# Kernel tuning notes

Measured on AMD Instinct MI355X. Metric: run time of the kernel, lower is better.

Reference implementation:

```python
import jax, jax.numpy as jnp
import numpy as np

N_NODES = 100000
N_EDGES = 3200000
IN_CH = 128
HID_CH = 128   # 2 * out_channels
OUT_CH = 64


def setup_inputs() -> dict:
    key = jax.random.key(0)
    ks = jax.random.split(key, 6)
    x = jax.random.normal(ks[0], (N_NODES, IN_CH), dtype=jnp.float32)
    edge_index = jax.random.randint(ks[1], (2, N_EDGES), 0, N_NODES, dtype=jnp.int64)
    # Glorot-ish init for GCN linear weights
    W1 = jax.random.normal(ks[2], (IN_CH, HID_CH), dtype=jnp.float32) / np.sqrt(IN_CH)
    b1 = jnp.zeros((HID_CH,), dtype=jnp.float32)
    W2 = jax.random.normal(ks[3], (HID_CH, OUT_CH), dtype=jnp.float32) / np.sqrt(HID_CH)
    b2 = jnp.zeros((OUT_CH,), dtype=jnp.float32)
    return {"x": x, "edge_index": edge_index, "W1": W1, "b1": b1, "W2": W2, "b2": b2}


def gcn_conv(x, src, dst, W, b, n):
    """PyG GCNConv: add self-loops, symmetric D^-1/2 (A+I) D^-1/2 normalization,
    linear transform, scatter-add aggregation, then bias."""
    h = x @ W  # [N, C_out]
    ones = jnp.ones(src.shape[0], dtype=x.dtype)
    deg = jax.ops.segment_sum(ones, dst, num_segments=n) + 1.0  # self-loop degree
    dinv = jax.lax.rsqrt(deg)  # [N]
    coef = dinv[src] * dinv[dst]  # [E] edge normalization
    agg = jax.ops.segment_sum(h[src] * coef[:, None], dst, num_segments=n)
    agg = agg + h * (dinv * dinv)[:, None]  # self-loop contribution
    return agg + b


def reference(x, edge_index, W1, b1, W2, b2):
    src, dst = edge_index[0], edge_index[1]
    n = x.shape[0]
    h = jax.nn.relu(gcn_conv(x, src, dst, W1, b1, n))
    out = jax.nn.relu(gcn_conv(h, src, dst, W2, b2, n))
    return out
```

## Files before the change

### kernel.cpp

```cpp
#include <hip/hip_runtime.h>
#include <hip/hip_fp16.h>
#include <cstdint>
#include <cstddef>


#define BSHIFT 8

typedef _Float16 half8 __attribute__((ext_vector_type(8)));
typedef float f32x4 __attribute__((ext_vector_type(4)));

__global__ __launch_bounds__(256) void k_hist(const int* __restrict__ dst,
                                              int* __restrict__ bkthist, int E) {
  __shared__ int h[512];
  for (int t = threadIdx.x; t < 512; t += 256) h[t] = 0;
  __syncthreads();
  int i = blockIdx.x * 256 + threadIdx.x;
  const int stride = gridDim.x * 256;
  for (; i < E; i += stride) atomicAdd(&h[dst[i] >> BSHIFT], 1);
  __syncthreads();
  for (int t = threadIdx.x; t < 512; t += 256)
    if (h[t]) atomicAdd(&bkthist[t], h[t]);
}

__global__ __launch_bounds__(256) void k_bktscan(const int* __restrict__ bkthist,
                                                 int* __restrict__ bktbase,
                                                 int* __restrict__ bktcur,
                                                 int* __restrict__ offsets, int n,
                                                 int E, int nbkt) {
  __shared__ int sc[512];
  const int t = threadIdx.x;
  sc[t] = (t < nbkt) ? bkthist[t] : 0;
  sc[256 + t] = (256 + t < nbkt) ? bkthist[256 + t] : 0;
  __syncthreads();
  if (t == 0) {
    int run = 0;
    for (int b = 0; b < nbkt; ++b) {
      const int c = sc[b];
      sc[b] = run;
      run += c;
    }
    offsets[n] = E;
    bktbase[nbkt] = E;
  }
  __syncthreads();
  if (t < nbkt) {
    bktbase[t] = sc[t];
    bktcur[t] = sc[t];
  }
  if (256 + t < nbkt) {
    bktbase[256 + t] = sc[256 + t];
    bktcur[256 + t] = sc[256 + t];
  }
}

__global__ __launch_bounds__(256) void k_part(const int* __restrict__ src,
                                              const int* __restrict__ dst,
                                              int* __restrict__ bktcur,
                                              int* __restrict__ part, int E,
                                              int nbkt) {
  __shared__ int hist[512];
  const int tid = threadIdx.x;
  const int e0 = blockIdx.x * 4096;
  for (int b = tid; b < nbkt; b += 256) hist[b] = 0;
  __syncthreads();
#pragma unroll
  for (int j = 0; j < 16; ++j) {
    const int e = e0 + j * 256 + tid;
    if (e < E) atomicAdd(&hist[dst[e] >> BSHIFT], 1);
  }
  __syncthreads();
  for (int b = tid; b < nbkt; b += 256) {
    const int c = hist[b];
    hist[b] = c ? atomicAdd(&bktcur[b], c) : 0;
  }
  __syncthreads();
#pragma unroll
  for (int j = 0; j < 16; ++j) {
    const int e = e0 + j * 256 + tid;
    if (e < E) {
      const int d = dst[e];
      const int pos = atomicAdd(&hist[d >> BSHIFT], 1);
      part[pos] = (src[e] << BSHIFT) | (d & ((1 << BSHIFT) - 1));
    }
  }
}

__global__ __launch_bounds__(256) void k_csr2(const int* __restrict__ part,
                                              const int* __restrict__ bktbase,
                                              int* __restrict__ offsets,
                                              int* __restrict__ csr_src,
                                              float* __restrict__ dinv, int n) {
  __shared__ int cnt[256];
  __shared__ int ts[256];
  const int b = blockIdx.x;
  const int node0 = b << BSHIFT;
  const int nn = min(256, n - node0);
  const int t = threadIdx.x;
  cnt[t] = 0;
  __syncthreads();
  const int w0 = bktbase[b];
  const int w1 = bktbase[b + 1];
  for (int e = w0 + t; e < w1; e += 256)
    atomicAdd(&cnt[part[e] & ((1 << BSHIFT) - 1)], 1);
  __syncthreads();
  const int c = cnt[t];
  ts[t] = c;
  __syncthreads();
  for (int off = 1; off < 256; off <<= 1) {
    const int u = (t >= off) ? ts[t - off] : 0;
    __syncthreads();
    ts[t] += u;
    __syncthreads();
  }
  const int excl = ts[t] - c;
  if (t < nn) {
    offsets[node0 + t] = w0 + excl;
    dinv[node0 + t] = rsqrtf((float)c + 1.0f);
  }
  cnt[t] = w0 + excl;
  __syncthreads();
  for (int e = w0 + t; e < w1; e += 256) {
    const int p = part[e];
    const int pos = atomicAdd(&cnt[p & ((1 << BSHIFT) - 1)], 1);
    csr_src[pos] = p >> BSHIFT;
  }
}

template <typename TA, int COLS>
__global__ __launch_bounds__(256) void k_gemm_mfma(const TA* __restrict__ A,
                                                   const float* __restrict__ W,
                                                   __half* __restrict__ Hout,
                                                   int N, int ntiles) {
  constexpr int RW = (COLS == 128) ? 2 : 4;
  constexpr int RPT = RW * 16;
  __shared__ _Float16 Wt[128 * COLS];
  __shared__ _Float16 Lb[4][16][72];
  const int tid = threadIdx.x;
  const int w = tid >> 6;
  const int l = tid & 63;

  for (int f = tid; f < (128 * COLS) / 4; f += 256) {
    const int k = f / (COLS / 4);
    const int c4 = (f % (COLS / 4)) * 4;
    const float4 wv = *reinterpret_cast<const float4*>(W + (size_t)k * COLS + c4);
#pragma unroll
    for (int j = 0; j < 4; ++j) {
      const int cc = c4 + j;
      Wt[(cc * 128 + k) ^ ((cc & 7) << 3)] = (_Float16)(&wv.x)[j];
    }
  }
  __syncthreads();

  const int colw = (COLS == 128) ? (w >> 1) * 64 : 0;
  const int rw = (COLS == 128) ? (w & 1) : w;
  const int koff = (l >> 4) * 8;

  half8 bf[4][4];
#pragma unroll
  for (int t = 0; t < 4; ++t)
#pragma unroll
    for (int s = 0; s < 4; ++s) {
      const int cc = colw + 16 * t + (l & 15);
      const int kk = 32 * s + koff;
      bf[t][s] =
          *reinterpret_cast<const half8*>(&Wt[(cc * 128 + kk) ^ ((cc & 7) << 3)]);
    }

  for (int tile = blockIdx.x; tile < ntiles; tile += gridDim.x) {
    const int row = tile * RPT + rw * 16 + (l & 15);
    const int rowc = (row < N) ? row : (N - 1);
    f32x4 acc[4];
#pragma unroll
    for (int t = 0; t < 4; ++t) acc[t] = (f32x4){0.f, 0.f, 0.f, 0.f};

#pragma unroll
    for (int s = 0; s < 4; ++s) {
      half8 af;
      if constexpr (sizeof(TA) == 4) {
        const float* ap = (const float*)A + (size_t)rowc * 128 + 32 * s + koff;
        const float4 a0 = *reinterpret_cast<const float4*>(ap);
        const float4 a1 = *reinterpret_cast<const float4*>(ap + 4);
#pragma unroll
        for (int j = 0; j < 4; ++j) {
          af[j] = (_Float16)(&a0.x)[j];
          af[4 + j] = (_Float16)(&a1.x)[j];
        }
      } else {
        af = *reinterpret_cast<const half8*>((const __half*)A +
                                             (size_t)rowc * 128 + 32 * s + koff);
      }
#pragma unroll
      for (int t = 0; t < 4; ++t)
        acc[t] = __builtin_amdgcn_mfma_f32_16x16x32_f16(af, bf[t][s], acc[t],
                                                        0, 0, 0);
    }

#pragma unroll
    for (int t = 0; t < 4; ++t)
#pragma unroll
      for (int r = 0; r < 4; ++r)
        Lb[w][(l >> 4) * 4 + r][16 * t + (l & 15)] = (_Float16)acc[t][r];
    const int orow = tile * RPT + rw * 16 + (l & 15);
    if (orow < N) {
      const int ch = (l >> 4) * 16;
      const half8 v0 = *reinterpret_cast<const half8*>(&Lb[w][l & 15][ch]);
      const half8 v1 = *reinterpret_cast<const half8*>(&Lb[w][l & 15][ch + 8]);
      __half* hp = Hout + (size_t)orow * COLS + colw + ch;
      *reinterpret_cast<half8*>(hp) = v0;
      *reinterpret_cast<half8*>(hp + 8) = v1;
    }
  }
}

__global__ __launch_bounds__(256) void k_gather128(
    const __half* __restrict__ H, const int* __restrict__ offsets,
    const int* __restrict__ csr_src, const float* __restrict__ dinv,
    const float* __restrict__ bias, float* __restrict__ out, int N) {
  const int lane = threadIdx.x & 63;
  const int g = lane >> 3;
  const int sl = lane & 7;
  int w = (blockIdx.x * 256 + threadIdx.x) >> 6;
  const int nw = (gridDim.x * 256) >> 6;
  for (int i = w; i < N; i += nw) {
    const float di = dinv[i];
    const int beg = offsets[i];
    const int end = offsets[i + 1];
    float acc[16];
    {
      const float cfs = (g == 0) ? di * di : 0.f;
      const float4 ha = *reinterpret_cast<const float4*>(H + (size_t)i * 128 + sl * 16);
      const float4 hb = *reinterpret_cast<const float4*>(H + (size_t)i * 128 + sl * 16 + 8);
      const __half2* hpa = reinterpret_cast<const __half2*>(&ha);
      const __half2* hpb = reinterpret_cast<const __half2*>(&hb);
#pragma unroll
      for (int q = 0; q < 4; ++q) {
        const float2 fa = __half22float2(hpa[q]);
        const float2 fb = __half22float2(hpb[q]);
        acc[q * 2] = cfs * fa.x;
        acc[q * 2 + 1] = cfs * fa.y;
        acc[8 + q * 2] = cfs * fb.x;
        acc[8 + q * 2 + 1] = cfs * fb.y;
      }
    }
    for (int base = beg; base < end; base += 8) {
      const int e = base + g;
      const bool v = e < end;
      const int s = v ? csr_src[e] : i;
      const float cf = v ? dinv[s] * di : 0.f;
      const float4 ha = *reinterpret_cast<const float4*>(H + (size_t)s * 128 + sl * 16);
      const float4 hb = *reinterpret_cast<const float4*>(H + (size_t)s * 128 + sl * 16 + 8);
      const __half2* hpa = reinterpret_cast<const __half2*>(&ha);
      const __half2* hpb = reinterpret_cast<const __half2*>(&hb);
#pragma unroll
      for (int q = 0; q < 4; ++q) {
        const float2 fa = __half22float2(hpa[q]);
        const float2 fb = __half22float2(hpb[q]);
        acc[q * 2] = fmaf(cf, fa.x, acc[q * 2]);
        acc[q * 2 + 1] = fmaf(cf, fa.y, acc[q * 2 + 1]);
        acc[8 + q * 2] = fmaf(cf, fb.x, acc[8 + q * 2]);
        acc[8 + q * 2 + 1] = fmaf(cf, fb.y, acc[8 + q * 2 + 1]);
      }
    }
#pragma unroll
    for (int j = 0; j < 16; ++j) {
      float a = acc[j];
      a += __shfl_xor(a, 8);
      a += __shfl_xor(a, 16);
      a += __shfl_xor(a, 32);
      acc[j] = a;
    }
    if (g == 0) {
      float* op = out + (size_t)i * 128 + sl * 16;
      const float4 b0 = *reinterpret_cast<const float4*>(bias + sl * 16);
      const float4 b1 = *reinterpret_cast<const float4*>(bias + sl * 16 + 4);
      const float4 b2 = *reinterpret_cast<const float4*>(bias + sl * 16 + 8);
      const float4 b3 = *reinterpret_cast<const float4*>(bias + sl * 16 + 12);
      float4 o;
      o.x = fmaxf(acc[0] + b0.x, 0.f);
      o.y = fmaxf(acc[1] + b0.y, 0.f);
      o.z = fmaxf(acc[2] + b0.z, 0.f);
      o.w = fmaxf(acc[3] + b0.w, 0.f);
      *reinterpret_cast<float4*>(op) = o;
      o.x = fmaxf(acc[4] + b1.x, 0.f);
      o.y = fmaxf(acc[5] + b1.y, 0.f);
      o.z = fmaxf(acc[6] + b1.z, 0.f);
      o.w = fmaxf(acc[7] + b1.w, 0.f);
      *reinterpret_cast<float4*>(op + 4) = o;
      o.x = fmaxf(acc[8] + b2.x, 0.f);
      o.y = fmaxf(acc[9] + b2.y, 0.f);
      o.z = fmaxf(acc[10] + b2.z, 0.f);
      o.w = fmaxf(acc[11] + b2.w, 0.f);
      *reinterpret_cast<float4*>(op + 8) = o;
      o.x = fmaxf(acc[12] + b3.x, 0.f);
      o.y = fmaxf(acc[13] + b3.y, 0.f);
      o.z = fmaxf(acc[14] + b3.z, 0.f);
      o.w = fmaxf(acc[15] + b3.w, 0.f);
      *reinterpret_cast<float4*>(op + 12) = o;
    }
  }
}

__global__ __launch_bounds__(256) void k_gather64(
    const __half* __restrict__ H, const int* __restrict__ offsets,
    const int* __restrict__ csr_src, const float* __restrict__ dinv,
    const float* __restrict__ bias, float* __restrict__ out, int N) {
  const int lane = threadIdx.x & 63;
  const int g = lane >> 3;
  const int sl = lane & 7;
  int w = (blockIdx.x * 256 + threadIdx.x) >> 6;
  const int nw = (gridDim.x * 256) >> 6;
  for (int i = w; i < N; i += nw) {
    const float di = dinv[i];
    const int beg = offsets[i];
    const int end = offsets[i + 1];
    float acc[8];
    {
      const float cfs = (g == 0) ? di * di : 0.f;
      const float4 ha = *reinterpret_cast<const float4*>(H + (size_t)i * 64 + sl * 8);
      const __half2* hpa = reinterpret_cast<const __half2*>(&ha);
#pragma unroll
      for (int q = 0; q < 4; ++q) {
        const float2 fa = __half22float2(hpa[q]);
        acc[q * 2] = cfs * fa.x;
        acc[q * 2 + 1] = cfs * fa.y;
      }
    }
    for (int base = beg; base < end; base += 8) {
      const int e = base + g;
      const bool v = e < end;
      const int s = v ? csr_src[e] : i;
      const float cf = v ? dinv[s] * di : 0.f;
      const float4 ha = *reinterpret_cast<const float4*>(H + (size_t)s * 64 + sl * 8);
      const __half2* hpa = reinterpret_cast<const __half2*>(&ha);
#pragma unroll
      for (int q = 0; q < 4; ++q) {
        const float2 fa = __half22float2(hpa[q]);
        acc[q * 2] = fmaf(cf, fa.x, acc[q * 2]);
        acc[q * 2 + 1] = fmaf(cf, fa.y, acc[q * 2 + 1]);
      }
    }
#pragma unroll
    for (int j = 0; j < 8; ++j) {
      float a = acc[j];
      a += __shfl_xor(a, 8);
      a += __shfl_xor(a, 16);
      a += __shfl_xor(a, 32);
      acc[j] = a;
    }
    if (g == 0) {
      float* op = out + (size_t)i * 64 + sl * 8;
      const float4 b0 = *reinterpret_cast<const float4*>(bias + sl * 8);
      const float4 b1 = *reinterpret_cast<const float4*>(bias + sl * 8 + 4);
      float4 o;
      o.x = fmaxf(acc[0] + b0.x, 0.f);
      o.y = fmaxf(acc[1] + b0.y, 0.f);
      o.z = fmaxf(acc[2] + b0.z, 0.f);
      o.w = fmaxf(acc[3] + b0.w, 0.f);
      *reinterpret_cast<float4*>(op) = o;
      o.x = fmaxf(acc[4] + b1.x, 0.f);
      o.y = fmaxf(acc[5] + b1.y, 0.f);
      o.z = fmaxf(acc[6] + b1.z, 0.f);
      o.w = fmaxf(acc[7] + b1.w, 0.f);
      *reinterpret_cast<float4*>(op + 4) = o;
    }
  }
}

extern "C" void kernel_launch(void* const* d_in, const int* in_sizes, int n_in,
                              void* d_out, int out_size, void* d_ws,
                              size_t ws_size, hipStream_t stream) {
  const float* x  = (const float*)d_in[0];
  const int*   ei = (const int*)d_in[1];
  const float* W1 = (const float*)d_in[2];
  const float* b1 = (const float*)d_in[3];
  const float* W2 = (const float*)d_in[4];
  const float* b2 = (const float*)d_in[5];

  const int IN  = 128;
  const int n   = in_sizes[0] / IN;
  const int E   = in_sizes[1] / 2;
  const int HID = in_sizes[2] / IN;
  const int* srcv = ei;
  const int* dstv = ei + E;
  float* out = (float*)d_out;

  const int NBKT = (n + 255) >> BSHIFT;
  const int NCHK = (E + 4095) / 4096;
  const int NT1  = (n + 31) / 32;
  const int NT2  = (n + 63) / 64;

  char* p = (char*)d_ws;
  auto take = [&](size_t bytes) {
    char* r = p;
    p += (bytes + 255) & ~(size_t)255;
    return r;
  };
  float*  dinv    = (float*)take((size_t)n * 4);
  int*    offsets = (int*)take((size_t)(n + 1) * 4);
  int*    bkthist = (int*)take(512 * 4);
  int*    bktbase = (int*)take(512 * 4);
  int*    bktcur  = (int*)take(512 * 4);
  int*    csr_src = (int*)take((size_t)E * 4);
  __half* H16     = (__half*)take((size_t)n * 128 * 2);
  float*  bufHp   = (float*)take((size_t)n * HID * 4);
  int*    part    = (int*)bufHp;

  hipMemsetAsync(bkthist, 0, 512 * 4, stream);
  k_hist<<<1024, 256, 0, stream>>>(dstv, bkthist, E);
  k_bktscan<<<1, 256, 0, stream>>>(bkthist, bktbase, bktcur, offsets, n, E, NBKT);
  k_part<<<NCHK, 256, 0, stream>>>(srcv, dstv, bktcur, part, E, NBKT);
  k_csr2<<<NBKT, 256, 0, stream>>>(part, bktbase, offsets, csr_src, dinv, n);

  k_gemm_mfma<float, 128><<<512, 256, 0, stream>>>(x, W1, H16, n, NT1);
  k_gather128<<<25000, 256, 0, stream>>>(H16, offsets, csr_src, dinv, b1,
                                         bufHp, n);

  k_gemm_mfma<float, 64><<<512, 256, 0, stream>>>(bufHp, W2, H16, n, NT2);
  k_gather64<<<25000, 256, 0, stream>>>(H16, offsets, csr_src, dinv, b2,
                                        out, n);
}
```

Baseline: 360.7 us.

## Slice H into column-sliced planes so gather blocks each touch one slice

```diff
diff --git a/kernel.cpp b/kernel.cpp
--- a/kernel.cpp
+++ b/kernel.cpp
@@ -8,6 +8,7 @@
 
 typedef _Float16 half8 __attribute__((ext_vector_type(8)));
 typedef float f32x4 __attribute__((ext_vector_type(4)));
+struct alignas(8) h4 { __half2 a, b; };
 
 __global__ __launch_bounds__(256) void k_hist(const int* __restrict__ dst,
                                               int* __restrict__ bkthist, int E) {
@@ -129,7 +130,7 @@
 template <typename TA, int COLS>
 __global__ __launch_bounds__(256) void k_gemm_mfma(const TA* __restrict__ A,
                                                    const float* __restrict__ W,
-                                                   __half* __restrict__ Hout,
+                                                   __half* __restrict__ Hs,
                                                    int N, int ntiles) {
   constexpr int RW = (COLS == 128) ? 2 : 4;
   constexpr int RPT = RW * 16;
@@ -205,163 +206,79 @@
       const int ch = (l >> 4) * 16;
       const half8 v0 = *reinterpret_cast<const half8*>(&Lb[w][l & 15][ch]);
       const half8 v1 = *reinterpret_cast<const half8*>(&Lb[w][l & 15][ch + 8]);
-      __half* hp = Hout + (size_t)orow * COLS + colw + ch;
-      *reinterpret_cast<half8*>(hp) = v0;
-      *reinterpret_cast<half8*>(hp + 8) = v1;
-    }
-  }
-}
-
-__global__ __launch_bounds__(256) void k_gather128(
-    const __half* __restrict__ H, const int* __restrict__ offsets,
+      const int cb = colw + ch;
+      if constexpr (COLS == 128) {
+        __half* hp = Hs + (size_t)(cb >> 4) * N * 16 + (size_t)orow * 16;
+        *reinterpret_cast<half8*>(hp) = v0;
+        *reinterpret_cast<half8*>(hp + 8) = v1;
+      } else {
+        __half* hp0 = Hs + (size_t)(cb >> 3) * N * 8 + (size_t)orow * 8;
+        __half* hp1 = Hs + (size_t)((cb >> 3) + 1) * N * 8 + (size_t)orow * 8;
+        *reinterpret_cast<half8*>(hp0) = v0;
+        *reinterpret_cast<half8*>(hp1) = v1;
+      }
+    }
+  }
+}
+
+template <int LPE, int COLS>
+__global__ __launch_bounds__(256) void k_gather_sl(
+    const __half* __restrict__ Hs, const int* __restrict__ offsets,
     const int* __restrict__ csr_src, const float* __restrict__ dinv,
     const float* __restrict__ bias, float* __restrict__ out, int N) {
+  constexpr int CH = LPE * 4;
+  constexpr int GPE = 64 / LPE;
+  const int sidx = blockIdx.x & 7;
+  const __half* Hb = Hs + (size_t)sidx * N * CH;
   const int lane = threadIdx.x & 63;
-  const int g = lane >> 3;
-  const int sl = lane & 7;
-  int w = (blockIdx.x * 256 + threadIdx.x) >> 6;
-  const int nw = (gridDim.x * 256) >> 6;
+  const int g = lane / LPE;
+  const int cl = lane % LPE;
+  const int c0 = sidx * CH + cl * 4;
+  int w = (blockIdx.x >> 3) * 4 + (threadIdx.x >> 6);
+  const int nw = (gridDim.x >> 3) * 4;
   for (int i = w; i < N; i += nw) {
     const float di = dinv[i];
     const int beg = offsets[i];
     const int end = offsets[i + 1];
-    float acc[16];
+    float acc[4];
     {
       const float cfs = (g == 0) ? di * di : 0.f;
-      const float4 ha = *reinterpret_cast<const float4*>(H + (size_t)i * 128 + sl * 16);
-      const float4 hb = *reinterpret_cast<const float4*>(H + (size_t)i * 128 + sl * 16 + 8);
-      const __half2* hpa = reinterpret_cast<const __half2*>(&ha);
-      const __half2* hpb = reinterpret_cast<const __half2*>(&hb);
-#pragma unroll
-      for (int q = 0; q < 4; ++q) {
-        const float2 fa = __half22float2(hpa[q]);
-        const float2 fb = __half22float2(hpb[q]);
-        acc[q * 2] = cfs * fa.x;
-        acc[q * 2 + 1] = cfs * fa.y;
-        acc[8 + q * 2] = cfs * fb.x;
-        acc[8 + q * 2 + 1] = cfs * fb.y;
-      }
-    }
-    for (int base = beg; base < end; base += 8) {
+      const h4 hv = *reinterpret_cast<const h4*>(Hb + (size_t)i * CH + cl * 4);
+      const float2 fa = __half22float2(hv.a);
+      const float2 fb = __half22float2(hv.b);
+      acc[0] = cfs * fa.x;
+      acc[1] = cfs * fa.y;
+      acc[2] = cfs * fb.x;
+      acc[3] = cfs * fb.y;
+    }
+    for (int base = beg; base < end; base += GPE) {
       const int e = base + g;
       const bool v = e < end;
-      const int s = v ? csr_src[e] : i;
+      const int s = v ? __builtin_nontemporal_load(csr_src + e) : i;
       const float cf = v ? dinv[s] * di : 0.f;
-      const float4 ha = *reinterpret_cast<const float4*>(H + (size_t)s * 128 + sl * 16);
-      const float4 hb = *reinterpret_cast<const float4*>(H + (size_t)s * 128 + sl * 16 + 8);
-      const __half2* hpa = reinterpret_cast<const __half2*>(&ha);
-      const __half2* hpb = reinterpret_cast<const __half2*>(&hb);
-#pragma unroll
-      for (int q = 0; q < 4; ++q) {
-        const float2 fa = __half22float2(hpa[q]);
-        const float2 fb = __half22float2(hpb[q]);
-        acc[q * 2] = fmaf(cf, fa.x, acc[q * 2]);
-        acc[q * 2 + 1] = fmaf(cf, fa.y, acc[q * 2 + 1]);
-        acc[8 + q * 2] = fmaf(cf, fb.x, acc[8 + q * 2]);
-        acc[8 + q * 2 + 1] = fmaf(cf, fb.y, acc[8 + q * 2 + 1]);
-      }
-    }
-#pragma unroll
-    for (int j = 0; j < 16; ++j) {
+      const h4 hv = *reinterpret_cast<const h4*>(Hb + (size_t)s * CH + cl * 4);
+      const float2 fa = __half22float2(hv.a);
+      const float2 fb = __half22float2(hv.b);
+      acc[0] = fmaf(cf, fa.x, acc[0]);
+      acc[1] = fmaf(cf, fa.y, acc[1]);
+      acc[2] = fmaf(cf, fb.x, acc[2]);
+      acc[3] = fmaf(cf, fb.y, acc[3]);
+    }
+#pragma unroll
+    for (int j = 0; j < 4; ++j) {
       float a = acc[j];
-      a += __shfl_xor(a, 8);
-      a += __shfl_xor(a, 16);
-      a += __shfl_xor(a, 32);
+#pragma unroll
+      for (int off = LPE; off < 64; off <<= 1) a += __shfl_xor(a, off);
       acc[j] = a;
     }
     if (g == 0) {
-      float* op = out + (size_t)i * 128 + sl * 16;
-      const float4 b0 = *reinterpret_cast<const float4*>(bias + sl * 16);
-      const float4 b1 = *reinterpret_cast<const float4*>(bias + sl * 16 + 4);
-      const float4 b2 = *reinterpret_cast<const float4*>(bias + sl * 16 + 8);
-      const float4 b3 = *reinterpret_cast<const float4*>(bias + sl * 16 + 12);
+      const float4 bv = *reinterpret_cast<const float4*>(bias + c0);
       float4 o;
-      o.x = fmaxf(acc[0] + b0.x, 0.f);
-      o.y = fmaxf(acc[1] + b0.y, 0.f);
-      o.z = fmaxf(acc[2] + b0.z, 0.f);
-      o.w = fmaxf(acc[3] + b0.w, 0.f);
-      *reinterpret_cast<float4*>(op) = o;
-      o.x = fmaxf(acc[4] + b1.x, 0.f);
-      o.y = fmaxf(acc[5] + b1.y, 0.f);
-      o.z = fmaxf(acc[6] + b1.z, 0.f);
-      o.w = fmaxf(acc[7] + b1.w, 0.f);
-      *reinterpret_cast<float4*>(op + 4) = o;
-      o.x = fmaxf(acc[8] + b2.x, 0.f);
-      o.y = fmaxf(acc[9] + b2.y, 0.f);
-      o.z = fmaxf(acc[10] + b2.z, 0.f);
-      o.w = fmaxf(acc[11] + b2.w, 0.f);
-      *reinterpret_cast<float4*>(op + 8) = o;
-      o.x = fmaxf(acc[12] + b3.x, 0.f);
-      o.y = fmaxf(acc[13] + b3.y, 0.f);
-      o.z = fmaxf(acc[14] + b3.z, 0.f);
-      o.w = fmaxf(acc[15] + b3.w, 0.f);
-      *reinterpret_cast<float4*>(op + 12) = o;
-    }
-  }
-}
-
-__global__ __launch_bounds__(256) void k_gather64(
-    const __half* __restrict__ H, const int* __restrict__ offsets,
-    const int* __restrict__ csr_src, const float* __restrict__ dinv,
-    const float* __restrict__ bias, float* __restrict__ out, int N) {
-  const int lane = threadIdx.x & 63;
-  const int g = lane >> 3;
-  const int sl = lane & 7;
-  int w = (blockIdx.x * 256 + threadIdx.x) >> 6;
-  const int nw = (gridDim.x * 256) >> 6;
-  for (int i = w; i < N; i += nw) {
-    const float di = dinv[i];
-    const int beg = offsets[i];
-    const int end = offsets[i + 1];
-    float acc[8];
-    {
-      const float cfs = (g == 0) ? di * di : 0.f;
-      const float4 ha = *reinterpret_cast<const float4*>(H + (size_t)i * 64 + sl * 8);
-      const __half2* hpa = reinterpret_cast<const __half2*>(&ha);
-#pragma unroll
-      for (int q = 0; q < 4; ++q) {
-        const float2 fa = __half22float2(hpa[q]);
-        acc[q * 2] = cfs * fa.x;
-        acc[q * 2 + 1] = cfs * fa.y;
-      }
-    }
-    for (int base = beg; base < end; base += 8) {
-      const int e = base + g;
-      const bool v = e < end;
-      const int s = v ? csr_src[e] : i;
-      const float cf = v ? dinv[s] * di : 0.f;
-      const float4 ha = *reinterpret_cast<const float4*>(H + (size_t)s * 64 + sl * 8);
-      const __half2* hpa = reinterpret_cast<const __half2*>(&ha);
-#pragma unroll
-      for (int q = 0; q < 4; ++q) {
-        const float2 fa = __half22float2(hpa[q]);
-        acc[q * 2] = fmaf(cf, fa.x, acc[q * 2]);
-        acc[q * 2 + 1] = fmaf(cf, fa.y, acc[q * 2 + 1]);
-      }
-    }
-#pragma unroll
-    for (int j = 0; j < 8; ++j) {
-      float a = acc[j];
-      a += __shfl_xor(a, 8);
-      a += __shfl_xor(a, 16);
-      a += __shfl_xor(a, 32);
-      acc[j] = a;
-    }
-    if (g == 0) {
-      float* op = out + (size_t)i * 64 + sl * 8;
-      const float4 b0 = *reinterpret_cast<const float4*>(bias + sl * 8);
-      const float4 b1 = *reinterpret_cast<const float4*>(bias + sl * 8 + 4);
-      float4 o;
-      o.x = fmaxf(acc[0] + b0.x, 0.f);
-      o.y = fmaxf(acc[1] + b0.y, 0.f);
-      o.z = fmaxf(acc[2] + b0.z, 0.f);
-      o.w = fmaxf(acc[3] + b0.w, 0.f);
-      *reinterpret_cast<float4*>(op) = o;
-      o.x = fmaxf(acc[4] + b1.x, 0.f);
-      o.y = fmaxf(acc[5] + b1.y, 0.f);
-      o.z = fmaxf(acc[6] + b1.z, 0.f);
-      o.w = fmaxf(acc[7] + b1.w, 0.f);
-      *reinterpret_cast<float4*>(op + 4) = o;
+      o.x = fmaxf(acc[0] + bv.x, 0.f);
+      o.y = fmaxf(acc[1] + bv.y, 0.f);
+      o.z = fmaxf(acc[2] + bv.z, 0.f);
+      o.w = fmaxf(acc[3] + bv.w, 0.f);
+      *reinterpret_cast<float4*>(out + (size_t)i * COLS + c0) = o;
     }
   }
 }
@@ -412,10 +329,10 @@
   k_csr2<<<NBKT, 256, 0, stream>>>(part, bktbase, offsets, csr_src, dinv, n);
 
   k_gemm_mfma<float, 128><<<512, 256, 0, stream>>>(x, W1, H16, n, NT1);
-  k_gather128<<<25000, 256, 0, stream>>>(H16, offsets, csr_src, dinv, b1,
-                                         bufHp, n);
+  k_gather_sl<4, 128><<<8192, 256, 0, stream>>>(H16, offsets, csr_src, dinv,
+                                                b1, bufHp, n);
 
   k_gemm_mfma<float, 64><<<512, 256, 0, stream>>>(bufHp, W2, H16, n, NT2);
-  k_gather64<<<25000, 256, 0, stream>>>(H16, offsets, csr_src, dinv, b2,
-                                        out, n);
-}
+  k_gather_sl<2, 64><<<8192, 256, 0, stream>>>(H16, offsets, csr_src, dinv,
+                                               b2, out, n);
+}
```

Result: slower. 985.9 us (+173.4%).

## Drop histogram pass via fixed-capacity buckets and store hidden activations in fp16

Applied to the files above, without the earlier changes.

```diff
diff --git a/kernel.cpp b/kernel.cpp
--- a/kernel.cpp
+++ b/kernel.cpp
@@ -5,52 +5,14 @@
 
 
 #define BSHIFT 8
+#define CAP    12288
 
 typedef _Float16 half8 __attribute__((ext_vector_type(8)));
 typedef float f32x4 __attribute__((ext_vector_type(4)));
 
-__global__ __launch_bounds__(256) void k_hist(const int* __restrict__ dst,
-                                              int* __restrict__ bkthist, int E) {
-  __shared__ int h[512];
-  for (int t = threadIdx.x; t < 512; t += 256) h[t] = 0;
-  __syncthreads();
-  int i = blockIdx.x * 256 + threadIdx.x;
-  const int stride = gridDim.x * 256;
-  for (; i < E; i += stride) atomicAdd(&h[dst[i] >> BSHIFT], 1);
-  __syncthreads();
-  for (int t = threadIdx.x; t < 512; t += 256)
-    if (h[t]) atomicAdd(&bkthist[t], h[t]);
-}
-
-__global__ __launch_bounds__(256) void k_bktscan(const int* __restrict__ bkthist,
-                                                 int* __restrict__ bktbase,
-                                                 int* __restrict__ bktcur,
-                                                 int* __restrict__ offsets, int n,
-                                                 int E, int nbkt) {
-  __shared__ int sc[512];
-  const int t = threadIdx.x;
-  sc[t] = (t < nbkt) ? bkthist[t] : 0;
-  sc[256 + t] = (256 + t < nbkt) ? bkthist[256 + t] : 0;
-  __syncthreads();
-  if (t == 0) {
-    int run = 0;
-    for (int b = 0; b < nbkt; ++b) {
-      const int c = sc[b];
-      sc[b] = run;
-      run += c;
-    }
-    offsets[n] = E;
-    bktbase[nbkt] = E;
-  }
-  __syncthreads();
-  if (t < nbkt) {
-    bktbase[t] = sc[t];
-    bktcur[t] = sc[t];
-  }
-  if (256 + t < nbkt) {
-    bktbase[256 + t] = sc[256 + t];
-    bktcur[256 + t] = sc[256 + t];
-  }
+__global__ __launch_bounds__(256) void k_binit(int* __restrict__ bktcur, int nbkt) {
+  int b = blockIdx.x * 256 + threadIdx.x;
+  if (b < nbkt) bktcur[b] = b * CAP;
 }
 
 __global__ __launch_bounds__(256) void k_part(const int* __restrict__ src,
@@ -79,13 +41,40 @@
     const int e = e0 + j * 256 + tid;
     if (e < E) {
       const int d = dst[e];
-      const int pos = atomicAdd(&hist[d >> BSHIFT], 1);
-      part[pos] = (src[e] << BSHIFT) | (d & ((1 << BSHIFT) - 1));
-    }
-  }
+      const int bkt = d >> BSHIFT;
+      const int pos = atomicAdd(&hist[bkt], 1);
+      if (pos < (bkt + 1) * CAP)
+        part[pos] = (src[e] << BSHIFT) | (d & ((1 << BSHIFT) - 1));
+    }
+  }
+}
+
+__global__ __launch_bounds__(256) void k_bktscan(const int* __restrict__ bktcur,
+                                                 int* __restrict__ bktbase,
+                                                 int* __restrict__ offsets, int n,
+                                                 int E, int nbkt) {
+  __shared__ int sc[512];
+  const int t = threadIdx.x;
+  sc[t] = (t < nbkt) ? (bktcur[t] - t * CAP) : 0;
+  sc[256 + t] = (256 + t < nbkt) ? (bktcur[256 + t] - (256 + t) * CAP) : 0;
+  __syncthreads();
+  if (t == 0) {
+    int run = 0;
+    for (int b = 0; b < nbkt; ++b) {
+      const int c = sc[b];
+      sc[b] = run;
+      run += c;
+    }
+    offsets[n] = E;
+    bktbase[nbkt] = E;
+  }
+  __syncthreads();
+  if (t < nbkt) bktbase[t] = sc[t];
+  if (256 + t < nbkt) bktbase[256 + t] = sc[256 + t];
 }
 
 __global__ __launch_bounds__(256) void k_csr2(const int* __restrict__ part,
+                                              const int* __restrict__ bktcur,
                                               const int* __restrict__ bktbase,
                                               int* __restrict__ offsets,
                                               int* __restrict__ csr_src,
@@ -98,9 +87,9 @@
   const int t = threadIdx.x;
   cnt[t] = 0;
   __syncthreads();
-  const int w0 = bktbase[b];
-  const int w1 = bktbase[b + 1];
-  for (int e = w0 + t; e < w1; e += 256)
+  const int w0p = b * CAP;
+  const int w1p = min(bktcur[b], w0p + CAP);
+  for (int e = w0p + t; e < w1p; e += 256)
     atomicAdd(&cnt[part[e] & ((1 << BSHIFT) - 1)], 1);
   __syncthreads();
   const int c = cnt[t];
@@ -113,13 +102,14 @@
     __syncthreads();
   }
   const int excl = ts[t] - c;
+  const int w0 = bktbase[b];
   if (t < nn) {
     offsets[node0 + t] = w0 + excl;
     dinv[node0 + t] = rsqrtf((float)c + 1.0f);
   }
   cnt[t] = w0 + excl;
   __syncthreads();
-  for (int e = w0 + t; e < w1; e += 256) {
+  for (int e = w0p + t; e < w1p; e += 256) {
     const int p = part[e];
     const int pos = atomicAdd(&cnt[p & ((1 << BSHIFT) - 1)], 1);
     csr_src[pos] = p >> BSHIFT;
@@ -215,7 +205,7 @@
 __global__ __launch_bounds__(256) void k_gather128(
     const __half* __restrict__ H, const int* __restrict__ offsets,
     const int* __restrict__ csr_src, const float* __restrict__ dinv,
-    const float* __restrict__ bias, float* __restrict__ out, int N) {
+    const float* __restrict__ bias, __half* __restrict__ out, int N) {
   const int lane = threadIdx.x & 63;
   const int g = lane >> 3;
   const int sl = lane & 7;
@@ -245,7 +235,7 @@
     for (int base = beg; base < end; base += 8) {
       const int e = base + g;
       const bool v = e < end;
-      const int s = v ? csr_src[e] : i;
+      const int s = v ? __builtin_nontemporal_load(csr_src + e) : i;
       const float cf = v ? dinv[s] * di : 0.f;
       const float4 ha = *reinterpret_cast<const float4*>(H + (size_t)s * 128 + sl * 16);
       const float4 hb = *reinterpret_cast<const float4*>(H + (size_t)s * 128 + sl * 16 + 8);
@@ -270,32 +260,16 @@
       acc[j] = a;
     }
     if (g == 0) {
-      float* op = out + (size_t)i * 128 + sl * 16;
-      const float4 b0 = *reinterpret_cast<const float4*>(bias + sl * 16);
-      const float4 b1 = *reinterpret_cast<const float4*>(bias + sl * 16 + 4);
-      const float4 b2 = *reinterpret_cast<const float4*>(bias + sl * 16 + 8);
-      const float4 b3 = *reinterpret_cast<const float4*>(bias + sl * 16 + 12);
-      float4 o;
-      o.x = fmaxf(acc[0] + b0.x, 0.f);
-      o.y = fmaxf(acc[1] + b0.y, 0.f);
-      o.z = fmaxf(acc[2] + b0.z, 0.f);
-      o.w = fmaxf(acc[3] + b0.w, 0.f);
-      *reinterpret_cast<float4*>(op) = o;
-      o.x = fmaxf(acc[4] + b1.x, 0.f);
-      o.y = fmaxf(acc[5] + b1.y, 0.f);
-      o.z = fmaxf(acc[6] + b1.z, 0.f);
-      o.w = fmaxf(acc[7] + b1.w, 0.f);
-      *reinterpret_cast<float4*>(op + 4) = o;
-      o.x = fmaxf(acc[8] + b2.x, 0.f);
-      o.y = fmaxf(acc[9] + b2.y, 0.f);
-      o.z = fmaxf(acc[10] + b2.z, 0.f);
-      o.w = fmaxf(acc[11] + b2.w, 0.f);
-      *reinterpret_cast<float4*>(op + 8) = o;
-      o.x = fmaxf(acc[12] + b3.x, 0.f);
-      o.y = fmaxf(acc[13] + b3.y, 0.f);
-      o.z = fmaxf(acc[14] + b3.z, 0.f);
-      o.w = fmaxf(acc[15] + b3.w, 0.f);
-      *reinterpret_cast<float4*>(op + 12) = o;
+      __half2 ov[8];
+#pragma unroll
+      for (int q = 0; q < 8; ++q) {
+        const float2 bv = *reinterpret_cast<const float2*>(bias + sl * 16 + q * 2);
+        ov[q] = __floats2half2_rn(fmaxf(acc[q * 2] + bv.x, 0.f),
+                                  fmaxf(acc[q * 2 + 1] + bv.y, 0.f));
+      }
+      __half* op = out + (size_t)i * 128 + sl * 16;
+      *reinterpret_cast<float4*>(op) = *reinterpret_cast<const float4*>(&ov[0]);
+      *reinterpret_cast<float4*>(op + 8) = *reinterpret_cast<const float4*>(&ov[4]);
     }
   }
 }
@@ -328,7 +302,7 @@
     for (int base = beg; base < end; base += 8) {
       const int e = base + g;
       const bool v = e < end;
-      const int s = v ? csr_src[e] : i;
+      const int s = v ? __builtin_nontemporal_load(csr_src + e) : i;
       const float cf = v ? dinv[s] * di : 0.f;
       const float4 ha = *reinterpret_cast<const float4*>(H + (size_t)s * 64 + sl * 8);
       const __half2* hpa = reinterpret_cast<const __half2*>(&ha);
@@ -379,7 +353,6 @@
   const int IN  = 128;
   const int n   = in_sizes[0] / IN;
   const int E   = in_sizes[1] / 2;
-  const int HID = in_sizes[2] / IN;
   const int* srcv = ei;
   const int* dstv = ei + E;
   float* out = (float*)d_out;
@@ -397,25 +370,24 @@
   };
   float*  dinv    = (float*)take((size_t)n * 4);
   int*    offsets = (int*)take((size_t)(n + 1) * 4);
-  int*    bkthist = (int*)take(512 * 4);
   int*    bktbase = (int*)take(512 * 4);
   int*    bktcur  = (int*)take(512 * 4);
   int*    csr_src = (int*)take((size_t)E * 4);
   __half* H16     = (__half*)take((size_t)n * 128 * 2);
-  float*  bufHp   = (float*)take((size_t)n * HID * 4);
-  int*    part    = (int*)bufHp;
-
-  hipMemsetAsync(bkthist, 0, 512 * 4, stream);
-  k_hist<<<1024, 256, 0, stream>>>(dstv, bkthist, E);
-  k_bktscan<<<1, 256, 0, stream>>>(bkthist, bktbase, bktcur, offsets, n, E, NBKT);
+  __half* hprime  = (__half*)take((size_t)n * 128 * 2);
+  int*    part    = (int*)hprime;
+
+  k_binit<<<(NBKT + 255) / 256, 256, 0, stream>>>(bktcur, NBKT);
   k_part<<<NCHK, 256, 0, stream>>>(srcv, dstv, bktcur, part, E, NBKT);
-  k_csr2<<<NBKT, 256, 0, stream>>>(part, bktbase, offsets, csr_src, dinv, n);
+  k_bktscan<<<1, 256, 0, stream>>>(bktcur, bktbase, offsets, n, E, NBKT);
+  k_csr2<<<NBKT, 256, 0, stream>>>(part, bktcur, bktbase, offsets, csr_src,
+                                   dinv, n);
 
   k_gemm_mfma<float, 128><<<512, 256, 0, stream>>>(x, W1, H16, n, NT1);
   k_gather128<<<25000, 256, 0, stream>>>(H16, offsets, csr_src, dinv, b1,
-                                         bufHp, n);
-
-  k_gemm_mfma<float, 64><<<512, 256, 0, stream>>>(bufHp, W2, H16, n, NT2);
+                                         hprime, n);
+
+  k_gemm_mfma<__half, 64><<<512, 256, 0, stream>>>(hprime, W2, H16, n, NT2);
   k_gather64<<<25000, 256, 0, stream>>>(H16, offsets, csr_src, dinv, b2,
                                         out, n);
 }
```

Measured after the change: 356.0 us. No clear change (-1.3%).
